# Kernel tuning notes

Hardware: AMD Instinct MI355X
Metric: run time of the kernel (lower is better)

## Reference

```python
import jax, jax.numpy as jnp
import numpy as np

N = 50000
E = 800000
IN_C = 128
HID_C = 128
OUT_C = 128
N_CLS = 40


def setup_inputs() -> dict:
    key = jax.random.key(0)
    ks = jax.random.split(key, 12)
    x = jax.random.normal(ks[0], (N, IN_C), dtype=jnp.float32)
    edge_index = jax.random.randint(ks[1], (2, E), 0, N, dtype=jnp.int64)
    s = 1.0 / np.sqrt(IN_C)
    W_l1 = jax.random.uniform(ks[2], (IN_C, HID_C), jnp.float32, -s, s)
    W_r1 = jax.random.uniform(ks[3], (IN_C, HID_C), jnp.float32, -s, s)
    b1 = jax.random.uniform(ks[4], (HID_C,), jnp.float32, -s, s)
    s2 = 1.0 / np.sqrt(HID_C)
    W_l2 = jax.random.uniform(ks[5], (HID_C, OUT_C), jnp.float32, -s2, s2)
    W_r2 = jax.random.uniform(ks[6], (HID_C, OUT_C), jnp.float32, -s2, s2)
    b2 = jax.random.uniform(ks[7], (OUT_C,), jnp.float32, -s2, s2)
    s3 = 1.0 / np.sqrt(OUT_C)
    W_c = jax.random.uniform(ks[8], (OUT_C, N_CLS), jnp.float32, -s3, s3)
    b_c = jax.random.uniform(ks[9], (N_CLS,), jnp.float32, -s3, s3)
    return {"x": x, "edge_index": edge_index, "W_l1": W_l1, "W_r1": W_r1,
            "b1": b1, "W_l2": W_l2, "W_r2": W_r2, "b2": b2,
            "W_c": W_c, "b_c": b_c}


def _mean_aggregate(x, src, dst, deg_inv):
    # gather source node features over edges, scatter-mean to dst nodes
    msg = x[src]  # [E, C]
    agg = jax.ops.segment_sum(msg, dst, num_segments=N)  # [N, C]
    return agg * deg_inv[:, None]


def _sage_conv(x, src, dst, deg_inv, W_l, W_r, b):
    # PyG SAGEConv (mean aggr): out = agg @ W_l + x @ W_r + b
    agg = _mean_aggregate(x, src, dst, deg_inv)
    return agg @ W_l + x @ W_r + b


def reference(x, edge_index, W_l1, W_r1, b1, W_l2, W_r2, b2, W_c, b_c):
    src, dst = edge_index[0], edge_index[1]
    deg = jax.ops.segment_sum(jnp.ones((E,), jnp.float32), dst, num_segments=N)
    deg_inv = jnp.where(deg > 0, 1.0 / jnp.maximum(deg, 1.0), 0.0)
    h = jax.nn.relu(_sage_conv(x, src, dst, deg_inv, W_l1, W_r1, b1))
    h = jax.nn.relu(_sage_conv(h, src, dst, deg_inv, W_l2, W_r2, b2))
    return h @ W_c + b_c
```

## Files before the change

### kernel.cpp

```cpp
#include <hip/hip_runtime.h>

#define N_NODES 50000
#define N_EDGES 800000
#define C 128
#define NCLS 40
#define KB 98
#define BCAP 9216

typedef short bf16x8 __attribute__((ext_vector_type(8)));
typedef float f32x4 __attribute__((ext_vector_type(4)));
typedef unsigned short ushort_t;

__device__ __forceinline__ unsigned short f32_to_bf16(float f) {
    union { float f; unsigned u; } c; c.f = f;
    unsigned r = (c.u + 0x7FFFu + ((c.u >> 16) & 1u)) >> 16;
    return (unsigned short)r;
}
__device__ __forceinline__ float bf_lo(unsigned u) {
    union { unsigned u; float f; } c; c.u = u << 16; return c.f;
}
__device__ __forceinline__ float bf_hi(unsigned u) {
    union { unsigned u; float f; } c; c.u = u & 0xffff0000u; return c.f;
}
__device__ __forceinline__ unsigned pack_bf16(float lo, float hi) {
    return (unsigned)f32_to_bf16(lo) | ((unsigned)f32_to_bf16(hi) << 16);
}

__global__ __launch_bounds__(256)
void convert_all(const float* __restrict__ Wl1, const float* __restrict__ Wr1,
                 const float* __restrict__ Wl2, const float* __restrict__ Wr2,
                 const float* __restrict__ Wc,  const float* __restrict__ x,
                 ushort_t* __restrict__ Wbf1, ushort_t* __restrict__ Wbf2,
                 ushort_t* __restrict__ Wcb,  ushort_t* __restrict__ xb) {
    int b = blockIdx.x;
    int tid = threadIdx.x;
    if (b < 256) {
        const float* Wl = (b < 128) ? Wl1 : Wl2;
        const float* Wr = (b < 128) ? Wr1 : Wr2;
        ushort_t* Bpre  = (b < 128) ? Wbf1 : Wbf2;
        int idx = (b & 127) * 256 + tid;
        int n = idx >> 8;
        int k = idx & 255;
        float v = (k < 128) ? Wl[k * 128 + n] : Wr[(k - 128) * 128 + n];
        Bpre[n * 256 + k] = f32_to_bf16(v);
    } else if (b < 280) {
        int idx = (b - 256) * 256 + tid;
        if (idx < 48 * 128) {
            int n = idx >> 7;
            int k = idx & 127;
            float v = (n < NCLS) ? Wc[k * NCLS + n] : 0.f;
            Wcb[idx] = f32_to_bf16(v);
        }
    } else {
        int idx = (b - 280) * 256 + tid;
        const float4 v0 = *(const float4*)&x[idx * 8];
        const float4 v1 = *(const float4*)&x[idx * 8 + 4];
        uint4 o;
        o.x = pack_bf16(v0.x, v0.y);
        o.y = pack_bf16(v0.z, v0.w);
        o.z = pack_bf16(v1.x, v1.y);
        o.w = pack_bf16(v1.z, v1.w);
        ((uint4*)xb)[idx] = o;
    }
}

__global__ __launch_bounds__(256)
void bin_kernel(const int* __restrict__ src, const int* __restrict__ dst,
                int* __restrict__ bucket_cnt, unsigned* __restrict__ bucket_data) {
    __shared__ int lh[KB];
    int tid = threadIdx.x;
    int e0 = blockIdx.x * 4096;
    if (tid < KB) lh[tid] = 0;
    __syncthreads();
#pragma unroll
    for (int j = 0; j < 16; ++j) {
        int e = e0 + j * 256 + tid;
        if (e < N_EDGES) atomicAdd(&lh[dst[e] >> 9], 1);
    }
    __syncthreads();
    if (tid < KB) lh[tid] = atomicAdd(&bucket_cnt[tid], lh[tid]);
    __syncthreads();
#pragma unroll
    for (int j = 0; j < 16; ++j) {
        int e = e0 + j * 256 + tid;
        if (e < N_EDGES) {
            int d = dst[e];
            int b = d >> 9;
            int pos = atomicAdd(&lh[b], 1);
            if (pos < BCAP)
                bucket_data[b * BCAP + pos] = (unsigned)src[e] | ((unsigned)(d & 511) << 16);
        }
    }
}

__global__ __launch_bounds__(256)
void build_kernel(const int* __restrict__ bucket_cnt, const unsigned* __restrict__ bucket_data,
                  int* __restrict__ row_ptr, ushort_t* __restrict__ csr16) {
    __shared__ int wt[4];
    __shared__ int wt2[4];
    __shared__ int sbases[128];
    __shared__ int hist[512];
    __shared__ int loff[512];
    __shared__ ushort_t lcsr[BCAP];
    int tid = threadIdx.x;
    int b = blockIdx.x;
    int n0 = b << 9;
    int nb = min(512, N_NODES - n0);

    int v = 0, x = 0;
    if (tid < 128) {
        v = (tid < KB) ? bucket_cnt[tid] : 0;
        x = v;
#pragma unroll
        for (int off = 1; off < 64; off <<= 1) {
            int t = __shfl_up(x, off, 64);
            if ((tid & 63) >= off) x += t;
        }
        if ((tid & 63) == 63) wt[tid >> 6] = x;
    }
    hist[tid] = 0; hist[tid + 256] = 0;
    __syncthreads();
    if (tid < 128) sbases[tid] = x - v + ((tid >= 64) ? wt[0] : 0);
    __syncthreads();
    int base = sbases[b];
    int ecnt = min(bucket_cnt[b], BCAP);

    for (int i = tid; i < ecnt; i += 256)
        atomicAdd(&hist[bucket_data[b * BCAP + i] >> 16], 1);
    __syncthreads();

    int h0 = hist[2 * tid], h1 = hist[2 * tid + 1];
    int s = h0 + h1;
    int y = s;
#pragma unroll
    for (int off = 1; off < 64; off <<= 1) {
        int t = __shfl_up(y, off, 64);
        if ((tid & 63) >= off) y += t;
    }
    if ((tid & 63) == 63) wt2[tid >> 6] = y;
    __syncthreads();
    int add = 0;
    for (int j = 0; j < (tid >> 6); ++j) add += wt2[j];
    int ex = y + add - s;
    loff[2 * tid] = ex;
    loff[2 * tid + 1] = ex + h0;
    __syncthreads();

    for (int n = tid; n < nb; n += 256) row_ptr[n0 + n] = base + loff[n];
    if (b == KB - 1 && tid == 0) row_ptr[N_NODES] = N_EDGES;
    __syncthreads();

    for (int i = tid; i < ecnt; i += 256) {
        unsigned e = bucket_data[b * BCAP + i];
        int pos = atomicAdd(&loff[e >> 16], 1);
        lcsr[pos] = (ushort_t)(e & 0xFFFFu);
    }
    __syncthreads();
    for (int i = tid; i < ecnt; i += 256) csr16[base + i] = lcsr[i];
}

#define ALD 136
template<int CLS>
__global__ __launch_bounds__(256)
void fused_layer(const ushort_t* __restrict__ feat,
                 const int* __restrict__ row_ptr,
                 const ushort_t* __restrict__ csr16,
                 const ushort_t* __restrict__ Bpre,
                 const float* __restrict__ bias,
                 ushort_t* __restrict__ hout,
                 const ushort_t* __restrict__ Wcb,
                 const float* __restrict__ bc,
                 float* __restrict__ out) {
    __shared__ ushort_t aggL[64 * ALD];
    __shared__ ushort_t stg[64 * 40 + 128 * 40];
    ushort_t* AsX = stg;
    ushort_t* BsP = stg + 64 * 40;
    const int tid = threadIdx.x;
    const int r0 = blockIdx.x * 64;
    const int w = tid >> 6, lane = tid & 63, m = lane & 15, quad = lane >> 4;

    const uint4* fb = (const uint4*)feat;
    const int q = tid & 15;
    for (int p = 0; p < 4; ++p) {
        int nl = p * 16 + (tid >> 4);
        int node = r0 + nl;
        int beg = 0, end = 0;
        if (node < N_NODES) { beg = row_ptr[node]; end = row_ptr[node + 1]; }
        float a0[8], a1[8], a2[8], a3[8];
#pragma unroll
        for (int j = 0; j < 8; ++j) { a0[j] = 0.f; a1[j] = 0.f; a2[j] = 0.f; a3[j] = 0.f; }
        int i = beg;
        for (; i + 4 <= end; i += 4) {
            int s0 = csr16[i + 0];
            int s1 = csr16[i + 1];
            int s2 = csr16[i + 2];
            int s3 = csr16[i + 3];
            uint4 v0 = fb[s0 * 16 + q];
            uint4 v1 = fb[s1 * 16 + q];
            uint4 v2 = fb[s2 * 16 + q];
            uint4 v3 = fb[s3 * 16 + q];
            a0[0] += bf_lo(v0.x); a0[1] += bf_hi(v0.x); a0[2] += bf_lo(v0.y); a0[3] += bf_hi(v0.y);
            a0[4] += bf_lo(v0.z); a0[5] += bf_hi(v0.z); a0[6] += bf_lo(v0.w); a0[7] += bf_hi(v0.w);
            a1[0] += bf_lo(v1.x); a1[1] += bf_hi(v1.x); a1[2] += bf_lo(v1.y); a1[3] += bf_hi(v1.y);
            a1[4] += bf_lo(v1.z); a1[5] += bf_hi(v1.z); a1[6] += bf_lo(v1.w); a1[7] += bf_hi(v1.w);
            a2[0] += bf_lo(v2.x); a2[1] += bf_hi(v2.x); a2[2] += bf_lo(v2.y); a2[3] += bf_hi(v2.y);
            a2[4] += bf_lo(v2.z); a2[5] += bf_hi(v2.z); a2[6] += bf_lo(v2.w); a2[7] += bf_hi(v2.w);
            a3[0] += bf_lo(v3.x); a3[1] += bf_hi(v3.x); a3[2] += bf_lo(v3.y); a3[3] += bf_hi(v3.y);
            a3[4] += bf_lo(v3.z); a3[5] += bf_hi(v3.z); a3[6] += bf_lo(v3.w); a3[7] += bf_hi(v3.w);
        }
        int rem = end - i;
        if (rem > 0) {
            int s0 = csr16[i];
            int s1 = csr16[i + (rem > 1 ? 1 : 0)];
            int s2 = csr16[i + (rem > 2 ? 2 : 0)];
            uint4 v0 = fb[s0 * 16 + q];
            uint4 v1 = fb[s1 * 16 + q];
            uint4 v2 = fb[s2 * 16 + q];
            float m1 = rem > 1 ? 1.f : 0.f;
            float m2 = rem > 2 ? 1.f : 0.f;
            a0[0] += bf_lo(v0.x); a0[1] += bf_hi(v0.x); a0[2] += bf_lo(v0.y); a0[3] += bf_hi(v0.y);
            a0[4] += bf_lo(v0.z); a0[5] += bf_hi(v0.z); a0[6] += bf_lo(v0.w); a0[7] += bf_hi(v0.w);
            a1[0] += m1 * bf_lo(v1.x); a1[1] += m1 * bf_hi(v1.x); a1[2] += m1 * bf_lo(v1.y); a1[3] += m1 * bf_hi(v1.y);
            a1[4] += m1 * bf_lo(v1.z); a1[5] += m1 * bf_hi(v1.z); a1[6] += m1 * bf_lo(v1.w); a1[7] += m1 * bf_hi(v1.w);
            a2[0] += m2 * bf_lo(v2.x); a2[1] += m2 * bf_hi(v2.x); a2[2] += m2 * bf_lo(v2.y); a2[3] += m2 * bf_hi(v2.y);
            a2[4] += m2 * bf_lo(v2.z); a2[5] += m2 * bf_hi(v2.z); a2[6] += m2 * bf_lo(v2.w); a2[7] += m2 * bf_hi(v2.w);
        }
        int d = end - beg;
        float di = d > 0 ? 1.f / (float)d : 0.f;
        float r[8];
#pragma unroll
        for (int j = 0; j < 8; ++j) r[j] = (a0[j] + a1[j] + a2[j] + a3[j]) * di;
        uint4 o;
        o.x = pack_bf16(r[0], r[1]);
        o.y = pack_bf16(r[2], r[3]);
        o.z = pack_bf16(r[4], r[5]);
        o.w = pack_bf16(r[6], r[7]);
        *(uint4*)&aggL[nl * ALD + q * 8] = o;
    }
    __syncthreads();

    f32x4 acc[8];
#pragma unroll
    for (int t = 0; t < 8; ++t) acc[t] = (f32x4){0.f, 0.f, 0.f, 0.f};

    for (int kc = 0; kc < 8; ++kc) {
        if (kc) __syncthreads();
        if (kc >= 4) {
            int row = tid >> 2;
            int kq = tid & 3;
            int rg = r0 + row; if (rg >= N_NODES) rg = N_NODES - 1;
            uint4 v = *(const uint4*)&feat[rg * C + (kc & 3) * 32 + kq * 8];
            *(uint4*)&AsX[row * 40 + kq * 8] = v;
        }
#pragma unroll
        for (int i = 0; i < 2; ++i) {
            int slot = tid + i * 256;
            int n = slot >> 2;
            int qq = slot & 3;
            *(uint4*)&BsP[n * 40 + qq * 8] = *(const uint4*)&Bpre[n * 256 + kc * 32 + qq * 8];
        }
        __syncthreads();
        bf16x8 af = (kc < 4)
            ? *(const bf16x8*)&aggL[(w * 16 + m) * ALD + kc * 32 + quad * 8]
            : *(const bf16x8*)&AsX[(w * 16 + m) * 40 + quad * 8];
#pragma unroll
        for (int t = 0; t < 8; ++t) {
            bf16x8 bf = *(const bf16x8*)&BsP[(t * 16 + m) * 40 + quad * 8];
            acc[t] = __builtin_amdgcn_mfma_f32_16x16x32_bf16(af, bf, acc[t], 0, 0, 0);
        }
    }

    if (CLS == 0) {
#pragma unroll
        for (int t = 0; t < 8; ++t) {
            int colv = t * 16 + m;
            float bv = bias[colv];
#pragma unroll
            for (int reg = 0; reg < 4; ++reg) {
                int rg = r0 + w * 16 + quad * 4 + reg;
                if (rg < N_NODES) {
                    float vv = fmaxf(acc[t][reg] + bv, 0.f);
                    hout[rg * C + colv] = f32_to_bf16(vv);
                }
            }
        }
    } else {
        __syncthreads();
#pragma unroll
        for (int t = 0; t < 8; ++t) {
            int colv = t * 16 + m;
            float bv = bias[colv];
#pragma unroll
            for (int reg = 0; reg < 4; ++reg) {
                int rl = w * 16 + quad * 4 + reg;
                float vv = fmaxf(acc[t][reg] + bv, 0.f);
                aggL[rl * ALD + colv] = f32_to_bf16(vv);
            }
        }
#pragma unroll
        for (int i = 0; i < 3; ++i) {
            int slot = tid + i * 256;
            int n = slot >> 4, kq = slot & 15;
            uint4 vv = *(const uint4*)&Wcb[n * C + kq * 8];
            *(uint4*)&stg[(kq >> 2) * (48 * 40) + n * 40 + (kq & 3) * 8] = vv;
        }
        __syncthreads();
        f32x4 acc2[3];
#pragma unroll
        for (int t = 0; t < 3; ++t) acc2[t] = (f32x4){0.f, 0.f, 0.f, 0.f};
#pragma unroll
        for (int kc = 0; kc < 4; ++kc) {
            bf16x8 af = *(const bf16x8*)&aggL[(w * 16 + m) * ALD + kc * 32 + quad * 8];
#pragma unroll
            for (int t = 0; t < 3; ++t) {
                bf16x8 bf = *(const bf16x8*)&stg[kc * (48 * 40) + (t * 16 + m) * 40 + quad * 8];
                acc2[t] = __builtin_amdgcn_mfma_f32_16x16x32_bf16(af, bf, acc2[t], 0, 0, 0);
            }
        }
#pragma unroll
        for (int t = 0; t < 3; ++t) {
            int col = t * 16 + m;
            if (col < NCLS) {
                float bvv = bc[col];
#pragma unroll
                for (int reg = 0; reg < 4; ++reg) {
                    int rg = r0 + w * 16 + quad * 4 + reg;
                    if (rg < N_NODES) out[rg * NCLS + col] = acc2[t][reg] + bvv;
                }
            }
        }
    }
}

extern "C" void kernel_launch(void* const* d_in, const int* in_sizes, int n_in,
                              void* d_out, int out_size, void* d_ws, size_t ws_size,
                              hipStream_t stream) {
    const float* x   = (const float*)d_in[0];
    const int*   ei  = (const int*)d_in[1];
    const float* Wl1 = (const float*)d_in[2];
    const float* Wr1 = (const float*)d_in[3];
    const float* b1  = (const float*)d_in[4];
    const float* Wl2 = (const float*)d_in[5];
    const float* Wr2 = (const float*)d_in[6];
    const float* b2  = (const float*)d_in[7];
    const float* Wc  = (const float*)d_in[8];
    const float* bc  = (const float*)d_in[9];
    const int* srcI = ei;
    const int* dstI = ei + N_EDGES;
    float* out = (float*)d_out;

    ushort_t* xb   = (ushort_t*)d_ws;
    ushort_t* h1b  = xb + (size_t)N_NODES * C;
    ushort_t* Wbf1 = h1b + (size_t)N_NODES * C;
    ushort_t* Wbf2 = Wbf1 + 32768;
    ushort_t* Wcb  = Wbf2 + 32768;
    ushort_t* csr16 = Wcb + 6144;
    int* bucket_cnt = (int*)(csr16 + N_EDGES);
    int* row_ptr    = bucket_cnt + 128;
    unsigned* bucket_data = (unsigned*)(row_ptr + N_NODES + 1);

    convert_all<<<280 + (N_NODES * C / 8 + 255) / 256, 256, 0, stream>>>(
        Wl1, Wr1, Wl2, Wr2, Wc, x, Wbf1, Wbf2, Wcb, xb);

    hipMemsetAsync(bucket_cnt, 0, 128 * sizeof(int), stream);
    bin_kernel<<<(N_EDGES + 4095) / 4096, 256, 0, stream>>>(srcI, dstI, bucket_cnt, bucket_data);
    build_kernel<<<KB, 256, 0, stream>>>(bucket_cnt, bucket_data, row_ptr, csr16);

    fused_layer<0><<<(N_NODES + 63) / 64, 256, 0, stream>>>(
        xb, row_ptr, csr16, Wbf1, b1, h1b, nullptr, nullptr, nullptr);

    fused_layer<1><<<(N_NODES + 63) / 64, 256, 0, stream>>>(
        h1b, row_ptr, csr16, Wbf2, b2, nullptr, Wcb, bc, out);
}
```

Before: 205.7 us.

## Split aggregation from GEMM, merge binning into convert kernel, widen CSR build

The binning pass is folded into the weight/feature conversion kernel, which removes one launch. The CSR build now runs with 512 threads so each thread owns one node. Each layer's fused gather+GEMM kernel is split into a standalone aggregation kernel, with 16 nodes per block for more parallelism, and a GEMM kernel. The GEMM kernel loads the full 64x256 A tile once and double-buffers the weight slices. The split adds an extra round trip of the aggregated features through global memory and two more launches, in exchange for better occupancy in the latency-bound gather.

```diff
diff --git a/kernel.cpp b/kernel.cpp
--- a/kernel.cpp
+++ b/kernel.cpp
@@ -6,6 +6,7 @@
 #define NCLS 40
 #define KB 98
 #define BCAP 9216
+#define NB_BIN 196
 
 typedef short bf16x8 __attribute__((ext_vector_type(8)));
 typedef float f32x4 __attribute__((ext_vector_type(4)));
@@ -27,24 +28,51 @@
 }
 
 __global__ __launch_bounds__(256)
-void convert_all(const float* __restrict__ Wl1, const float* __restrict__ Wr1,
-                 const float* __restrict__ Wl2, const float* __restrict__ Wr2,
-                 const float* __restrict__ Wc,  const float* __restrict__ x,
-                 ushort_t* __restrict__ Wbf1, ushort_t* __restrict__ Wbf2,
-                 ushort_t* __restrict__ Wcb,  ushort_t* __restrict__ xb) {
+void front_kernel(const int* __restrict__ src, const int* __restrict__ dst,
+                  int* __restrict__ bucket_cnt, unsigned* __restrict__ bucket_data,
+                  const float* __restrict__ Wl1, const float* __restrict__ Wr1,
+                  const float* __restrict__ Wl2, const float* __restrict__ Wr2,
+                  const float* __restrict__ Wc,  const float* __restrict__ x,
+                  ushort_t* __restrict__ Wbf1, ushort_t* __restrict__ Wbf2,
+                  ushort_t* __restrict__ Wcb,  ushort_t* __restrict__ xb) {
+    __shared__ int lh[KB];
     int b = blockIdx.x;
     int tid = threadIdx.x;
-    if (b < 256) {
-        const float* Wl = (b < 128) ? Wl1 : Wl2;
-        const float* Wr = (b < 128) ? Wr1 : Wr2;
-        ushort_t* Bpre  = (b < 128) ? Wbf1 : Wbf2;
-        int idx = (b & 127) * 256 + tid;
+    if (b < NB_BIN) {
+        int e0 = b * 4096;
+        if (tid < KB) lh[tid] = 0;
+        __syncthreads();
+#pragma unroll
+        for (int j = 0; j < 16; ++j) {
+            int e = e0 + j * 256 + tid;
+            if (e < N_EDGES) atomicAdd(&lh[dst[e] >> 9], 1);
+        }
+        __syncthreads();
+        if (tid < KB) lh[tid] = atomicAdd(&bucket_cnt[tid], lh[tid]);
+        __syncthreads();
+#pragma unroll
+        for (int j = 0; j < 16; ++j) {
+            int e = e0 + j * 256 + tid;
+            if (e < N_EDGES) {
+                int d = dst[e];
+                int bk = d >> 9;
+                int pos = atomicAdd(&lh[bk], 1);
+                if (pos < BCAP)
+                    bucket_data[bk * BCAP + pos] = (unsigned)src[e] | ((unsigned)(d & 511) << 16);
+            }
+        }
+    } else if (b < NB_BIN + 256) {
+        int bb = b - NB_BIN;
+        const float* Wl = (bb < 128) ? Wl1 : Wl2;
+        const float* Wr = (bb < 128) ? Wr1 : Wr2;
+        ushort_t* Bpre  = (bb < 128) ? Wbf1 : Wbf2;
+        int idx = (bb & 127) * 256 + tid;
         int n = idx >> 8;
         int k = idx & 255;
         float v = (k < 128) ? Wl[k * 128 + n] : Wr[(k - 128) * 128 + n];
         Bpre[n * 256 + k] = f32_to_bf16(v);
-    } else if (b < 280) {
-        int idx = (b - 256) * 256 + tid;
+    } else if (b < NB_BIN + 280) {
+        int idx = (b - (NB_BIN + 256)) * 256 + tid;
         if (idx < 48 * 128) {
             int n = idx >> 7;
             int k = idx & 127;
@@ -52,7 +80,7 @@
             Wcb[idx] = f32_to_bf16(v);
         }
     } else {
-        int idx = (b - 280) * 256 + tid;
+        int idx = (b - (NB_BIN + 280)) * 256 + tid;
         const float4 v0 = *(const float4*)&x[idx * 8];
         const float4 v1 = *(const float4*)&x[idx * 8 + 4];
         uint4 o;
@@ -64,40 +92,11 @@
     }
 }
 
-__global__ __launch_bounds__(256)
-void bin_kernel(const int* __restrict__ src, const int* __restrict__ dst,
-                int* __restrict__ bucket_cnt, unsigned* __restrict__ bucket_data) {
-    __shared__ int lh[KB];
-    int tid = threadIdx.x;
-    int e0 = blockIdx.x * 4096;
-    if (tid < KB) lh[tid] = 0;
-    __syncthreads();
-#pragma unroll
-    for (int j = 0; j < 16; ++j) {
-        int e = e0 + j * 256 + tid;
-        if (e < N_EDGES) atomicAdd(&lh[dst[e] >> 9], 1);
-    }
-    __syncthreads();
-    if (tid < KB) lh[tid] = atomicAdd(&bucket_cnt[tid], lh[tid]);
-    __syncthreads();
-#pragma unroll
-    for (int j = 0; j < 16; ++j) {
-        int e = e0 + j * 256 + tid;
-        if (e < N_EDGES) {
-            int d = dst[e];
-            int b = d >> 9;
-            int pos = atomicAdd(&lh[b], 1);
-            if (pos < BCAP)
-                bucket_data[b * BCAP + pos] = (unsigned)src[e] | ((unsigned)(d & 511) << 16);
-        }
-    }
-}
-
-__global__ __launch_bounds__(256)
+__global__ __launch_bounds__(512)
 void build_kernel(const int* __restrict__ bucket_cnt, const unsigned* __restrict__ bucket_data,
                   int* __restrict__ row_ptr, ushort_t* __restrict__ csr16) {
     __shared__ int wt[4];
-    __shared__ int wt2[4];
+    __shared__ int wt2[8];
     __shared__ int sbases[128];
     __shared__ int hist[512];
     __shared__ int loff[512];
@@ -107,31 +106,30 @@
     int n0 = b << 9;
     int nb = min(512, N_NODES - n0);
 
-    int v = 0, x = 0;
+    int v = 0, xs = 0;
     if (tid < 128) {
         v = (tid < KB) ? bucket_cnt[tid] : 0;
-        x = v;
+        xs = v;
 #pragma unroll
         for (int off = 1; off < 64; off <<= 1) {
-            int t = __shfl_up(x, off, 64);
-            if ((tid & 63) >= off) x += t;
-        }
-        if ((tid & 63) == 63) wt[tid >> 6] = x;
-    }
-    hist[tid] = 0; hist[tid + 256] = 0;
-    __syncthreads();
-    if (tid < 128) sbases[tid] = x - v + ((tid >= 64) ? wt[0] : 0);
+            int t = __shfl_up(xs, off, 64);
+            if ((tid & 63) >= off) xs += t;
+        }
+        if ((tid & 63) == 63) wt[tid >> 6] = xs;
+    }
+    hist[tid] = 0;
+    __syncthreads();
+    if (tid < 128) sbases[tid] = xs - v + ((tid >= 64) ? wt[0] : 0);
     __syncthreads();
     int base = sbases[b];
     int ecnt = min(bucket_cnt[b], BCAP);
 
-    for (int i = tid; i < ecnt; i += 256)
+    for (int i = tid; i < ecnt; i += 512)
         atomicAdd(&hist[bucket_data[b * BCAP + i] >> 16], 1);
     __syncthreads();
 
-    int h0 = hist[2 * tid], h1 = hist[2 * tid + 1];
-    int s = h0 + h1;
-    int y = s;
+    int h = hist[tid];
+    int y = h;
 #pragma unroll
     for (int off = 1; off < 64; off <<= 1) {
         int t = __shfl_up(y, off, 64);
@@ -141,101 +139,115 @@
     __syncthreads();
     int add = 0;
     for (int j = 0; j < (tid >> 6); ++j) add += wt2[j];
-    int ex = y + add - s;
-    loff[2 * tid] = ex;
-    loff[2 * tid + 1] = ex + h0;
-    __syncthreads();
-
-    for (int n = tid; n < nb; n += 256) row_ptr[n0 + n] = base + loff[n];
+    int ex = y + add - h;
+    loff[tid] = ex;
+    __syncthreads();
+
+    if (tid < nb) row_ptr[n0 + tid] = base + ex;
     if (b == KB - 1 && tid == 0) row_ptr[N_NODES] = N_EDGES;
-    __syncthreads();
-
-    for (int i = tid; i < ecnt; i += 256) {
+
+    for (int i = tid; i < ecnt; i += 512) {
         unsigned e = bucket_data[b * BCAP + i];
         int pos = atomicAdd(&loff[e >> 16], 1);
         lcsr[pos] = (ushort_t)(e & 0xFFFFu);
     }
     __syncthreads();
-    for (int i = tid; i < ecnt; i += 256) csr16[base + i] = lcsr[i];
-}
-
-#define ALD 136
+    for (int i = tid; i < ecnt; i += 512) csr16[base + i] = lcsr[i];
+}
+
+__global__ __launch_bounds__(256)
+void aggregate_bf16(const ushort_t* __restrict__ feat,
+                    const int* __restrict__ row_ptr,
+                    const ushort_t* __restrict__ csr16,
+                    ushort_t* __restrict__ agg) {
+    int tid = threadIdx.x;
+    int node = blockIdx.x * 16 + (tid >> 4);
+    int q = tid & 15;
+    if (node >= N_NODES) return;
+    const uint4* fb = (const uint4*)feat;
+    int beg = row_ptr[node];
+    int end = row_ptr[node + 1];
+    float a0[8], a1[8], a2[8], a3[8];
+#pragma unroll
+    for (int j = 0; j < 8; ++j) { a0[j] = 0.f; a1[j] = 0.f; a2[j] = 0.f; a3[j] = 0.f; }
+    int i = beg;
+    for (; i + 4 <= end; i += 4) {
+        int s0 = csr16[i + 0];
+        int s1 = csr16[i + 1];
+        int s2 = csr16[i + 2];
+        int s3 = csr16[i + 3];
+        uint4 v0 = fb[s0 * 16 + q];
+        uint4 v1 = fb[s1 * 16 + q];
+        uint4 v2 = fb[s2 * 16 + q];
+        uint4 v3 = fb[s3 * 16 + q];
+        a0[0] += bf_lo(v0.x); a0[1] += bf_hi(v0.x); a0[2] += bf_lo(v0.y); a0[3] += bf_hi(v0.y);
+        a0[4] += bf_lo(v0.z); a0[5] += bf_hi(v0.z); a0[6] += bf_lo(v0.w); a0[7] += bf_hi(v0.w);
+        a1[0] += bf_lo(v1.x); a1[1] += bf_hi(v1.x); a1[2] += bf_lo(v1.y); a1[3] += bf_hi(v1.y);
+        a1[4] += bf_lo(v1.z); a1[5] += bf_hi(v1.z); a1[6] += bf_lo(v1.w); a1[7] += bf_hi(v1.w);
+        a2[0] += bf_lo(v2.x); a2[1] += bf_hi(v2.x); a2[2] += bf_lo(v2.y); a2[3] += bf_hi(v2.y);
+        a2[4] += bf_lo(v2.z); a2[5] += bf_hi(v2.z); a2[6] += bf_lo(v2.w); a2[7] += bf_hi(v2.w);
+        a3[0] += bf_lo(v3.x); a3[1] += bf_hi(v3.x); a3[2] += bf_lo(v3.y); a3[3] += bf_hi(v3.y);
+        a3[4] += bf_lo(v3.z); a3[5] += bf_hi(v3.z); a3[6] += bf_lo(v3.w); a3[7] += bf_hi(v3.w);
+    }
+    int rem = end - i;
+    if (rem > 0) {
+        int s0 = csr16[i];
+        int s1 = csr16[i + (rem > 1 ? 1 : 0)];
+        int s2 = csr16[i + (rem > 2 ? 2 : 0)];
+        uint4 v0 = fb[s0 * 16 + q];
+        uint4 v1 = fb[s1 * 16 + q];
+        uint4 v2 = fb[s2 * 16 + q];
+        float m1 = rem > 1 ? 1.f : 0.f;
+        float m2 = rem > 2 ? 1.f : 0.f;
+        a0[0] += bf_lo(v0.x); a0[1] += bf_hi(v0.x); a0[2] += bf_lo(v0.y); a0[3] += bf_hi(v0.y);
+        a0[4] += bf_lo(v0.z); a0[5] += bf_hi(v0.z); a0[6] += bf_lo(v0.w); a0[7] += bf_hi(v0.w);
+        a1[0] += m1 * bf_lo(v1.x); a1[1] += m1 * bf_hi(v1.x); a1[2] += m1 * bf_lo(v1.y); a1[3] += m1 * bf_hi(v1.y);
+        a1[4] += m1 * bf_lo(v1.z); a1[5] += m1 * bf_hi(v1.z); a1[6] += m1 * bf_lo(v1.w); a1[7] += m1 * bf_hi(v1.w);
+        a2[0] += m2 * bf_lo(v2.x); a2[1] += m2 * bf_hi(v2.x); a2[2] += m2 * bf_lo(v2.y); a2[3] += m2 * bf_hi(v2.y);
+        a2[4] += m2 * bf_lo(v2.z); a2[5] += m2 * bf_hi(v2.z); a2[6] += m2 * bf_lo(v2.w); a2[7] += m2 * bf_hi(v2.w);
+    }
+    int d = end - beg;
+    float di = d > 0 ? 1.f / (float)d : 0.f;
+    float r[8];
+#pragma unroll
+    for (int j = 0; j < 8; ++j) r[j] = (a0[j] + a1[j] + a2[j] + a3[j]) * di;
+    uint4 o;
+    o.x = pack_bf16(r[0], r[1]);
+    o.y = pack_bf16(r[2], r[3]);
+    o.z = pack_bf16(r[4], r[5]);
+    o.w = pack_bf16(r[6], r[7]);
+    ((uint4*)agg)[node * 16 + q] = o;
+}
+
+#define ATS 264
 template<int CLS>
 __global__ __launch_bounds__(256)
-void fused_layer(const ushort_t* __restrict__ feat,
-                 const int* __restrict__ row_ptr,
-                 const ushort_t* __restrict__ csr16,
-                 const ushort_t* __restrict__ Bpre,
-                 const float* __restrict__ bias,
-                 ushort_t* __restrict__ hout,
-                 const ushort_t* __restrict__ Wcb,
-                 const float* __restrict__ bc,
-                 float* __restrict__ out) {
-    __shared__ ushort_t aggL[64 * ALD];
-    __shared__ ushort_t stg[64 * 40 + 128 * 40];
-    ushort_t* AsX = stg;
-    ushort_t* BsP = stg + 64 * 40;
+void gemm_layer(const ushort_t* __restrict__ aggb, const ushort_t* __restrict__ feat,
+                const ushort_t* __restrict__ Bpre, const float* __restrict__ bias,
+                ushort_t* __restrict__ hout,
+                const ushort_t* __restrict__ Wcb, const float* __restrict__ bc,
+                float* __restrict__ out) {
+    __shared__ ushort_t At[64 * ATS];
+    __shared__ ushort_t Bs[2][128 * 40];
     const int tid = threadIdx.x;
     const int r0 = blockIdx.x * 64;
     const int w = tid >> 6, lane = tid & 63, m = lane & 15, quad = lane >> 4;
 
-    const uint4* fb = (const uint4*)feat;
-    const int q = tid & 15;
-    for (int p = 0; p < 4; ++p) {
-        int nl = p * 16 + (tid >> 4);
-        int node = r0 + nl;
-        int beg = 0, end = 0;
-        if (node < N_NODES) { beg = row_ptr[node]; end = row_ptr[node + 1]; }
-        float a0[8], a1[8], a2[8], a3[8];
-#pragma unroll
-        for (int j = 0; j < 8; ++j) { a0[j] = 0.f; a1[j] = 0.f; a2[j] = 0.f; a3[j] = 0.f; }
-        int i = beg;
-        for (; i + 4 <= end; i += 4) {
-            int s0 = csr16[i + 0];
-            int s1 = csr16[i + 1];
-            int s2 = csr16[i + 2];
-            int s3 = csr16[i + 3];
-            uint4 v0 = fb[s0 * 16 + q];
-            uint4 v1 = fb[s1 * 16 + q];
-            uint4 v2 = fb[s2 * 16 + q];
-            uint4 v3 = fb[s3 * 16 + q];
-            a0[0] += bf_lo(v0.x); a0[1] += bf_hi(v0.x); a0[2] += bf_lo(v0.y); a0[3] += bf_hi(v0.y);
-            a0[4] += bf_lo(v0.z); a0[5] += bf_hi(v0.z); a0[6] += bf_lo(v0.w); a0[7] += bf_hi(v0.w);
-            a1[0] += bf_lo(v1.x); a1[1] += bf_hi(v1.x); a1[2] += bf_lo(v1.y); a1[3] += bf_hi(v1.y);
-            a1[4] += bf_lo(v1.z); a1[5] += bf_hi(v1.z); a1[6] += bf_lo(v1.w); a1[7] += bf_hi(v1.w);
-            a2[0] += bf_lo(v2.x); a2[1] += bf_hi(v2.x); a2[2] += bf_lo(v2.y); a2[3] += bf_hi(v2.y);
-            a2[4] += bf_lo(v2.z); a2[5] += bf_hi(v2.z); a2[6] += bf_lo(v2.w); a2[7] += bf_hi(v2.w);
-            a3[0] += bf_lo(v3.x); a3[1] += bf_hi(v3.x); a3[2] += bf_lo(v3.y); a3[3] += bf_hi(v3.y);
-            a3[4] += bf_lo(v3.z); a3[5] += bf_hi(v3.z); a3[6] += bf_lo(v3.w); a3[7] += bf_hi(v3.w);
-        }
-        int rem = end - i;
-        if (rem > 0) {
-            int s0 = csr16[i];
-            int s1 = csr16[i + (rem > 1 ? 1 : 0)];
-            int s2 = csr16[i + (rem > 2 ? 2 : 0)];
-            uint4 v0 = fb[s0 * 16 + q];
-            uint4 v1 = fb[s1 * 16 + q];
-            uint4 v2 = fb[s2 * 16 + q];
-            float m1 = rem > 1 ? 1.f : 0.f;
-            float m2 = rem > 2 ? 1.f : 0.f;
-            a0[0] += bf_lo(v0.x); a0[1] += bf_hi(v0.x); a0[2] += bf_lo(v0.y); a0[3] += bf_hi(v0.y);
-            a0[4] += bf_lo(v0.z); a0[5] += bf_hi(v0.z); a0[6] += bf_lo(v0.w); a0[7] += bf_hi(v0.w);
-            a1[0] += m1 * bf_lo(v1.x); a1[1] += m1 * bf_hi(v1.x); a1[2] += m1 * bf_lo(v1.y); a1[3] += m1 * bf_hi(v1.y);
-            a1[4] += m1 * bf_lo(v1.z); a1[5] += m1 * bf_hi(v1.z); a1[6] += m1 * bf_lo(v1.w); a1[7] += m1 * bf_hi(v1.w);
-            a2[0] += m2 * bf_lo(v2.x); a2[1] += m2 * bf_hi(v2.x); a2[2] += m2 * bf_lo(v2.y); a2[3] += m2 * bf_hi(v2.y);
-            a2[4] += m2 * bf_lo(v2.z); a2[5] += m2 * bf_hi(v2.z); a2[6] += m2 * bf_lo(v2.w); a2[7] += m2 * bf_hi(v2.w);
-        }
-        int d = end - beg;
-        float di = d > 0 ? 1.f / (float)d : 0.f;
-        float r[8];
-#pragma unroll
-        for (int j = 0; j < 8; ++j) r[j] = (a0[j] + a1[j] + a2[j] + a3[j]) * di;
-        uint4 o;
-        o.x = pack_bf16(r[0], r[1]);
-        o.y = pack_bf16(r[2], r[3]);
-        o.z = pack_bf16(r[4], r[5]);
-        o.w = pack_bf16(r[6], r[7]);
-        *(uint4*)&aggL[nl * ALD + q * 8] = o;
+    const uint4* au = (const uint4*)aggb;
+    const uint4* fu = (const uint4*)feat;
+#pragma unroll
+    for (int i = 0; i < 8; ++i) {
+        int slot = tid + i * 256;
+        int row = slot >> 5, u = slot & 31;
+        int rg = r0 + row; if (rg >= N_NODES) rg = N_NODES - 1;
+        uint4 vv = (u < 16) ? au[rg * 16 + u] : fu[rg * 16 + (u - 16)];
+        *(uint4*)&At[row * ATS + u * 8] = vv;
+    }
+#pragma unroll
+    for (int i = 0; i < 2; ++i) {
+        int slot = tid + i * 256;
+        int n = slot >> 2, qq = slot & 3;
+        *(uint4*)&Bs[0][n * 40 + qq * 8] = *(const uint4*)&Bpre[n * 256 + qq * 8];
     }
     __syncthreads();
 
@@ -244,30 +256,22 @@
     for (int t = 0; t < 8; ++t) acc[t] = (f32x4){0.f, 0.f, 0.f, 0.f};
 
     for (int kc = 0; kc < 8; ++kc) {
-        if (kc) __syncthreads();
-        if (kc >= 4) {
-            int row = tid >> 2;
-            int kq = tid & 3;
-            int rg = r0 + row; if (rg >= N_NODES) rg = N_NODES - 1;
-            uint4 v = *(const uint4*)&feat[rg * C + (kc & 3) * 32 + kq * 8];
-            *(uint4*)&AsX[row * 40 + kq * 8] = v;
-        }
-#pragma unroll
-        for (int i = 0; i < 2; ++i) {
-            int slot = tid + i * 256;
-            int n = slot >> 2;
-            int qq = slot & 3;
-            *(uint4*)&BsP[n * 40 + qq * 8] = *(const uint4*)&Bpre[n * 256 + kc * 32 + qq * 8];
-        }
-        __syncthreads();
-        bf16x8 af = (kc < 4)
-            ? *(const bf16x8*)&aggL[(w * 16 + m) * ALD + kc * 32 + quad * 8]
-            : *(const bf16x8*)&AsX[(w * 16 + m) * 40 + quad * 8];
+        if (kc < 7) {
+#pragma unroll
+            for (int i = 0; i < 2; ++i) {
+                int slot = tid + i * 256;
+                int n = slot >> 2, qq = slot & 3;
+                *(uint4*)&Bs[(kc + 1) & 1][n * 40 + qq * 8] =
+                    *(const uint4*)&Bpre[n * 256 + (kc + 1) * 32 + qq * 8];
+            }
+        }
+        bf16x8 af = *(const bf16x8*)&At[(w * 16 + m) * ATS + kc * 32 + quad * 8];
 #pragma unroll
         for (int t = 0; t < 8; ++t) {
-            bf16x8 bf = *(const bf16x8*)&BsP[(t * 16 + m) * 40 + quad * 8];
+            bf16x8 bf = *(const bf16x8*)&Bs[kc & 1][(t * 16 + m) * 40 + quad * 8];
             acc[t] = __builtin_amdgcn_mfma_f32_16x16x32_bf16(af, bf, acc[t], 0, 0, 0);
         }
+        __syncthreads();
     }
 
     if (CLS == 0) {
@@ -285,7 +289,6 @@
             }
         }
     } else {
-        __syncthreads();
 #pragma unroll
         for (int t = 0; t < 8; ++t) {
             int colv = t * 16 + m;
@@ -294,15 +297,16 @@
             for (int reg = 0; reg < 4; ++reg) {
                 int rl = w * 16 + quad * 4 + reg;
                 float vv = fmaxf(acc[t][reg] + bv, 0.f);
-                aggL[rl * ALD + colv] = f32_to_bf16(vv);
-            }
-        }
+                At[rl * ATS + colv] = f32_to_bf16(vv);
+            }
+        }
+        ushort_t* wcs = &Bs[0][0];
 #pragma unroll
         for (int i = 0; i < 3; ++i) {
             int slot = tid + i * 256;
             int n = slot >> 4, kq = slot & 15;
             uint4 vv = *(const uint4*)&Wcb[n * C + kq * 8];
-            *(uint4*)&stg[(kq >> 2) * (48 * 40) + n * 40 + (kq & 3) * 8] = vv;
+            *(uint4*)&wcs[(kq >> 2) * (48 * 40) + n * 40 + (kq & 3) * 8] = vv;
         }
         __syncthreads();
         f32x4 acc2[3];
@@ -310,10 +314,10 @@
         for (int t = 0; t < 3; ++t) acc2[t] = (f32x4){0.f, 0.f, 0.f, 0.f};
 #pragma unroll
         for (int kc = 0; kc < 4; ++kc) {
-            bf16x8 af = *(const bf16x8*)&aggL[(w * 16 + m) * ALD + kc * 32 + quad * 8];
+            bf16x8 af = *(const bf16x8*)&At[(w * 16 + m) * ATS + kc * 32 + quad * 8];
 #pragma unroll
             for (int t = 0; t < 3; ++t) {
-                bf16x8 bf = *(const bf16x8*)&stg[kc * (48 * 40) + (t * 16 + m) * 40 + quad * 8];
+                bf16x8 bf = *(const bf16x8*)&wcs[kc * (48 * 40) + (t * 16 + m) * 40 + quad * 8];
                 acc2[t] = __builtin_amdgcn_mfma_f32_16x16x32_bf16(af, bf, acc2[t], 0, 0, 0);
             }
         }
@@ -351,7 +355,8 @@
 
     ushort_t* xb   = (ushort_t*)d_ws;
     ushort_t* h1b  = xb + (size_t)N_NODES * C;
-    ushort_t* Wbf1 = h1b + (size_t)N_NODES * C;
+    ushort_t* aggb = h1b + (size_t)N_NODES * C;
+    ushort_t* Wbf1 = aggb + (size_t)N_NODES * C;
     ushort_t* Wbf2 = Wbf1 + 32768;
     ushort_t* Wcb  = Wbf2 + 32768;
     ushort_t* csr16 = Wcb + 6144;
@@ -359,16 +364,18 @@
     int* row_ptr    = bucket_cnt + 128;
     unsigned* bucket_data = (unsigned*)(row_ptr + N_NODES + 1);
 
-    convert_all<<<280 + (N_NODES * C / 8 + 255) / 256, 256, 0, stream>>>(
+    hipMemsetAsync(bucket_cnt, 0, 128 * sizeof(int), stream);
+    front_kernel<<<NB_BIN + 280 + (N_NODES * C / 8) / 256, 256, 0, stream>>>(
+        srcI, dstI, bucket_cnt, bucket_data,
         Wl1, Wr1, Wl2, Wr2, Wc, x, Wbf1, Wbf2, Wcb, xb);
 
-    hipMemsetAsync(bucket_cnt, 0, 128 * sizeof(int), stream);
-    bin_kernel<<<(N_EDGES + 4095) / 4096, 256, 0, stream>>>(srcI, dstI, bucket_cnt, bucket_data);
-    build_kernel<<<KB, 256, 0, stream>>>(bucket_cnt, bucket_data, row_ptr, csr16);
-
-    fused_layer<0><<<(N_NODES + 63) / 64, 256, 0, stream>>>(
-        xb, row_ptr, csr16, Wbf1, b1, h1b, nullptr, nullptr, nullptr);
-
-    fused_layer<1><<<(N_NODES + 63) / 64, 256, 0, stream>>>(
-        h1b, row_ptr, csr16, Wbf2, b2, nullptr, Wcb, bc, out);
-}
+    build_kernel<<<KB, 512, 0, stream>>>(bucket_cnt, bucket_data, row_ptr, csr16);
+
+    aggregate_bf16<<<(N_NODES + 15) / 16, 256, 0, stream>>>(xb, row_ptr, csr16, aggb);
+    gemm_layer<0><<<(N_NODES + 63) / 64, 256, 0, stream>>>(
+        aggb, xb, Wbf1, b1, h1b, nullptr, nullptr, nullptr);
+
+    aggregate_bf16<<<(N_NODES + 15) / 16, 256, 0, stream>>>(h1b, row_ptr, csr16, aggb);
+    gemm_layer<1><<<(N_NODES + 63) / 64, 256, 0, stream>>>(
+        aggb, h1b, Wbf2, b2, nullptr, Wcb, bc, out);
+}
```

Result: slower. 212.2 us (+3.2%).
